# Optimization experiments

Hardware: AMD Instinct MI355X
Metric: run time of the kernel (lower is better)

## Reference

```python
import jax, jax.numpy as jnp
import numpy as np

B, DIM_IN, DIM_OUT, NUM_X = 1024, 256, 256, 64
X_MIN, X_MAX = -2.0, 2.0


def setup_inputs() -> dict:
    key = jax.random.key(0)
    k1, k2 = jax.random.split(key)
    x = jax.random.normal(k1, (B, DIM_IN), dtype=jnp.float32)
    # xavier_uniform_ on Y [dim_in, dim_out, num_x]:
    # fan_in = dim_out*num_x, fan_out = dim_in*num_x
    bound = float(np.sqrt(6.0 / (DIM_OUT * NUM_X + DIM_IN * NUM_X)))
    Y = jax.random.uniform(k2, (DIM_IN, DIM_OUT, NUM_X), dtype=jnp.float32,
                           minval=-bound, maxval=bound)
    X = jnp.linspace(X_MIN, X_MAX, NUM_X, dtype=jnp.float32)
    return {"x": x, "X": X, "Y": Y}


def reference(x, X, Y):
    # x: [B, I], X: [K] sorted grid, Y: [I, J, K]
    K = X.shape[0]
    # bucket search: interval index such that X[idx-1] <= x < X[idx],
    # clipped so out-of-range points extrapolate linearly from edge segment
    idx = jnp.clip(jnp.searchsorted(X, x, side="right"), 1, K - 1)  # [B, I]
    x0 = X[idx - 1]
    x1 = X[idx]
    t = (x - x0) / (x1 - x0)  # [B, I]
    # sparse interpolation weights over grid points: [B, I, K]
    w = (1.0 - t)[..., None] * jax.nn.one_hot(idx - 1, K, dtype=x.dtype) \
        + t[..., None] * jax.nn.one_hot(idx, K, dtype=x.dtype)
    # out[b, j] = sum_i sum_k w[b,i,k] * Y[i,j,k]  (fuses lerp-gather + dim_in reduce)
    return jnp.einsum("bik,ijk->bj", w, Y)
```

## Files before the change

kernel.cpp:

```cpp
#include <hip/hip_runtime.h>
#include <hip/hip_bf16.h>

#define B_N   1024
#define DIM_I 256
#define DIM_J 256
#define NUM_K 64

__global__ __launch_bounds__(256) void kan_transpose(const float* __restrict__ Y,
                                                     unsigned short* __restrict__ Y2) {
    __shared__ float lds[64][65];
    const int i  = blockIdx.x >> 2;
    const int j0 = (blockIdx.x & 3) << 6;
    const float* src = Y + (size_t)(i * DIM_J + j0) * NUM_K;

    for (int e = threadIdx.x; e < 4096; e += 256) {
        int jl = e >> 6, k = e & 63;
        lds[jl][k] = src[e];
    }
    __syncthreads();
    for (int e = threadIdx.x; e < 4096; e += 256) {
        int kl = e >> 6, jl = e & 63;
        unsigned bits = __float_as_uint(lds[jl][kl]);
        unsigned r = bits + 0x7FFFu + ((bits >> 16) & 1u);
        Y2[(size_t)(i * NUM_K + kl) * DIM_J + j0 + jl] = (unsigned short)(r >> 16);
    }
}

__global__ __launch_bounds__(128) void kan_main(const float* __restrict__ x,
                                                const float* __restrict__ Xg,
                                                const unsigned short* __restrict__ Y2,
                                                float* __restrict__ out) {
    __shared__ float Xs[NUM_K];
    __shared__ int   offs[DIM_I];
    __shared__ float ts[DIM_I];

    const int b = blockIdx.x;
    const int t = threadIdx.x;

    if (t < NUM_K) Xs[t] = Xg[t];
    __syncthreads();

    for (int e = t; e < DIM_I; e += 128) {
        float xv = x[b * DIM_I + e];
        int m = (int)floorf((xv + 2.0f) * (63.0f / 4.0f)) + 1;
        m = m < 1 ? 1 : (m > 63 ? 63 : m);
        while (m < 63 && Xs[m] <= xv) ++m;
        while (m > 1 && Xs[m - 1] > xv) --m;
        float x0 = Xs[m - 1], x1 = Xs[m];
        ts[e]   = (xv - x0) / (x1 - x0);
        offs[e] = (e * NUM_K + (m - 1)) * DIM_J;
    }
    __syncthreads();

    const int jp = t << 1;
    float acc0 = 0.f, acc1 = 0.f;
    #pragma unroll 8
    for (int i = 0; i < DIM_I; ++i) {
        int   o  = offs[i];
        float tt = ts[i];
        unsigned pa = *reinterpret_cast<const unsigned*>(Y2 + o + jp);
        unsigned pb = *reinterpret_cast<const unsigned*>(Y2 + o + DIM_J + jp);
        float a0 = __uint_as_float(pa << 16);
        float a1 = __uint_as_float(pa & 0xFFFF0000u);
        float b0 = __uint_as_float(pb << 16);
        float b1 = __uint_as_float(pb & 0xFFFF0000u);
        acc0 += a0; acc0 = fmaf(tt, b0 - a0, acc0);
        acc1 += a1; acc1 = fmaf(tt, b1 - a1, acc1);
    }

    out[b * DIM_J + jp]     = acc0;
    out[b * DIM_J + jp + 1] = acc1;
}

extern "C" void kernel_launch(void* const* d_in, const int* in_sizes, int n_in,
                              void* d_out, int out_size, void* d_ws, size_t ws_size,
                              hipStream_t stream) {
    const float* x  = (const float*)d_in[0];
    const float* Xg = (const float*)d_in[1];
    const float* Y  = (const float*)d_in[2];
    float* out = (float*)d_out;
    unsigned short* Y2 = (unsigned short*)d_ws;

    kan_transpose<<<B_N, 256, 0, stream>>>(Y, Y2);
    kan_main<<<B_N, 128, 0, stream>>>(x, Xg, Y2, out);
}
```

Measured before the change: 91.41 us.

## Pack adjacent grid values per word and split dim_in reduction across blocks

The packing kernel now stores each bf16 grid value together with its next-k neighbour in one 32-bit word, so the main loop does a single 8-byte load per i instead of two separate 4-byte loads. The main kernel splits the dim_in reduction into four chunks across four times as many blocks to raise parallelism, and writes partial sums that a new reduce kernel combines. The lerp is rewritten as two FMAs with a precomputed (1-t). The cost is a workspace twice as large (32 MB packed), an extra 4 MB partials round trip and a third kernel launch.

```diff
diff --git a/kernel.cpp b/kernel.cpp
--- a/kernel.cpp
+++ b/kernel.cpp
@@ -1,75 +1,88 @@
 #include <hip/hip_runtime.h>
-#include <hip/hip_bf16.h>
 
-#define B_N   1024
-#define DIM_I 256
-#define DIM_J 256
-#define NUM_K 64
+#define B_N    1024
+#define DIM_I  256
+#define DIM_J  256
+#define NUM_K  64
+#define CHUNKS 4
+#define I_PER  (DIM_I / CHUNKS)
 
-__global__ __launch_bounds__(256) void kan_transpose(const float* __restrict__ Y,
-                                                     unsigned short* __restrict__ Y2) {
+__device__ __forceinline__ unsigned bf16bits(float f) {
+    unsigned b = __float_as_uint(f);
+    return (b + 0x7FFFu + ((b >> 16) & 1u)) >> 16;
+}
+
+__global__ __launch_bounds__(256) void kan_pack(const float* __restrict__ Y,
+                                                unsigned* __restrict__ Y3) {
     __shared__ float lds[64][65];
     const int i  = blockIdx.x >> 2;
     const int j0 = (blockIdx.x & 3) << 6;
     const float* src = Y + (size_t)(i * DIM_J + j0) * NUM_K;
 
-    for (int e = threadIdx.x; e < 4096; e += 256) {
-        int jl = e >> 6, k = e & 63;
-        lds[jl][k] = src[e];
-    }
+    for (int e = threadIdx.x; e < 4096; e += 256)
+        lds[e >> 6][e & 63] = src[e];
     __syncthreads();
     for (int e = threadIdx.x; e < 4096; e += 256) {
         int kl = e >> 6, jl = e & 63;
-        unsigned bits = __float_as_uint(lds[jl][kl]);
-        unsigned r = bits + 0x7FFFu + ((bits >> 16) & 1u);
-        Y2[(size_t)(i * NUM_K + kl) * DIM_J + j0 + jl] = (unsigned short)(r >> 16);
+        float v0 = lds[jl][kl];
+        float v1 = (kl < 63) ? lds[jl][kl + 1] : 0.0f;
+        Y3[(i * NUM_K + kl) * DIM_J + j0 + jl] = bf16bits(v0) | (bf16bits(v1) << 16);
     }
 }
 
 __global__ __launch_bounds__(128) void kan_main(const float* __restrict__ x,
                                                 const float* __restrict__ Xg,
-                                                const unsigned short* __restrict__ Y2,
-                                                float* __restrict__ out) {
-    __shared__ float Xs[NUM_K];
-    __shared__ int   offs[DIM_I];
-    __shared__ float ts[DIM_I];
+                                                const unsigned* __restrict__ Y3,
+                                                float* __restrict__ part) {
+    __shared__ float  Xs[NUM_K];
+    __shared__ float2 ot[I_PER];
 
-    const int b = blockIdx.x;
+    const int b = blockIdx.x >> 2;
+    const int c = blockIdx.x & 3;
     const int t = threadIdx.x;
 
     if (t < NUM_K) Xs[t] = Xg[t];
     __syncthreads();
 
-    for (int e = t; e < DIM_I; e += 128) {
-        float xv = x[b * DIM_I + e];
+    if (t < I_PER) {
+        const int i = c * I_PER + t;
+        float xv = x[b * DIM_I + i];
         int m = (int)floorf((xv + 2.0f) * (63.0f / 4.0f)) + 1;
         m = m < 1 ? 1 : (m > 63 ? 63 : m);
         while (m < 63 && Xs[m] <= xv) ++m;
         while (m > 1 && Xs[m - 1] > xv) --m;
         float x0 = Xs[m - 1], x1 = Xs[m];
-        ts[e]   = (xv - x0) / (x1 - x0);
-        offs[e] = (e * NUM_K + (m - 1)) * DIM_J;
+        float tt = (xv - x0) / (x1 - x0);
+        int off = (i * NUM_K + (m - 1)) * DIM_J;
+        ot[t] = make_float2(tt, __int_as_float(off));
     }
     __syncthreads();
 
     const int jp = t << 1;
     float acc0 = 0.f, acc1 = 0.f;
     #pragma unroll 8
-    for (int i = 0; i < DIM_I; ++i) {
-        int   o  = offs[i];
-        float tt = ts[i];
-        unsigned pa = *reinterpret_cast<const unsigned*>(Y2 + o + jp);
-        unsigned pb = *reinterpret_cast<const unsigned*>(Y2 + o + DIM_J + jp);
-        float a0 = __uint_as_float(pa << 16);
-        float a1 = __uint_as_float(pa & 0xFFFF0000u);
-        float b0 = __uint_as_float(pb << 16);
-        float b1 = __uint_as_float(pb & 0xFFFF0000u);
-        acc0 += a0; acc0 = fmaf(tt, b0 - a0, acc0);
-        acc1 += a1; acc1 = fmaf(tt, b1 - a1, acc1);
+    for (int i = 0; i < I_PER; ++i) {
+        float2 o  = ot[i];
+        float  tt = o.x;
+        float  s  = 1.0f - tt;
+        int    off = __float_as_int(o.y);
+        uint2  p  = *reinterpret_cast<const uint2*>(Y3 + off + jp);
+        float a0 = __uint_as_float(p.x << 16);
+        float b0 = __uint_as_float(p.x & 0xFFFF0000u);
+        float a1 = __uint_as_float(p.y << 16);
+        float b1 = __uint_as_float(p.y & 0xFFFF0000u);
+        acc0 = fmaf(s, a0, acc0); acc0 = fmaf(tt, b0, acc0);
+        acc1 = fmaf(s, a1, acc1); acc1 = fmaf(tt, b1, acc1);
     }
+    *reinterpret_cast<float2*>(part + ((c << 10) + b) * DIM_J + jp)
+        = make_float2(acc0, acc1);
+}
 
-    out[b * DIM_J + jp]     = acc0;
-    out[b * DIM_J + jp + 1] = acc1;
+__global__ __launch_bounds__(256) void kan_reduce(const float* __restrict__ part,
+                                                  float* __restrict__ out) {
+    const int idx = blockIdx.x * 256 + threadIdx.x;
+    const int BJ = B_N * DIM_J;
+    out[idx] = (part[idx] + part[BJ + idx]) + (part[2 * BJ + idx] + part[3 * BJ + idx]);
 }
 
 extern "C" void kernel_launch(void* const* d_in, const int* in_sizes, int n_in,
@@ -79,8 +92,11 @@
     const float* Xg = (const float*)d_in[1];
     const float* Y  = (const float*)d_in[2];
     float* out = (float*)d_out;
-    unsigned short* Y2 = (unsigned short*)d_ws;
 
-    kan_transpose<<<B_N, 256, 0, stream>>>(Y, Y2);
-    kan_main<<<B_N, 128, 0, stream>>>(x, Xg, Y2, out);
+    unsigned* Y3  = (unsigned*)d_ws;
+    float*    prt = (float*)((char*)d_ws + (32u << 20));
+
+    kan_pack  <<<B_N,            256, 0, stream>>>(Y, Y3);
+    kan_main  <<<B_N * CHUNKS,   128, 0, stream>>>(x, Xg, Y3, prt);
+    kan_reduce<<<B_N,            256, 0, stream>>>(prt, out);
 }
```

Measured after the change: 94.53 us. 1.03x slower.
